# Performance work log

Measured on AMD Instinct MI355X. Metric: run time of the kernel, lower is better.

Reference implementation:

```python
import jax, jax.numpy as jnp
import numpy as np

B, M, E, K = 8, 256, 128, 16
H, A, R, RMS = 1024, 256, 1024, 512
NEG = -1e25


def setup_inputs() -> dict:
    key = jax.random.key(0)
    ks = jax.random.split(key, 12)
    inp = {
        "mention_reprs": jax.random.normal(ks[0], (B, M, H), jnp.float32),
        "entities": jax.random.randint(ks[1], (B, E, K), 0, M),
        "entity_masks": jax.random.randint(ks[2], (B, E, K), 0, 2, dtype=jnp.int32),
        "relation_memory": jax.random.normal(ks[3], (R, RMS), jnp.float32),
        # GatedMILAttention params
        "Wv": jax.random.normal(ks[4], (A, H), jnp.float32) / np.sqrt(H),
        "bv": jnp.zeros((A,), jnp.float32),
        "Wu": jax.random.normal(ks[5], (A, H), jnp.float32) / np.sqrt(H),
        "bu": jnp.zeros((A,), jnp.float32),
        "Wa": jax.random.normal(ks[6], (1, A), jnp.float32) / np.sqrt(A),
        "ba": jnp.zeros((1,), jnp.float32),
        # relation memory read linear: Linear(RMS, H)
        "Wr": jax.random.normal(ks[7], (H, RMS), jnp.float32) / np.sqrt(RMS),
        "br": jnp.zeros((H,), jnp.float32),
        # output linear: Linear(H + RMS, H)
        "Wo": jax.random.normal(ks[8], (H, H + RMS), jnp.float32) / np.sqrt(H + RMS),
        "bo": jnp.zeros((H,), jnp.float32),
    }
    return inp


def reference(mention_reprs, entities, entity_masks, relation_memory,
              Wv, bv, Wu, bu, Wa, ba, Wr, br, Wo, bo):
    # gather mention clusters: [B, E, K, H]
    clusters = jax.vmap(lambda m, e: m[e])(mention_reprs, entities)
    # gated MIL attention
    aV = jnp.tanh(jnp.einsum('bekh,ah->beka', clusters, Wv) + bv)
    aU = jax.nn.sigmoid(jnp.einsum('bekh,ah->beka', clusters, Wu) + bu)
    logits = jnp.einsum('beka,oa->beko', aV * aU, Wa) + ba  # [B,E,K,1]
    mask = entity_masks[..., None].astype(bool)
    logits = jnp.where(mask, logits, NEG)
    a = jax.nn.softmax(logits, axis=2)
    # weighted pooling over mentions: [B, E, H]
    entity_reprs = jnp.sum(a * clusters, axis=2)
    # relation memory read (memory detached for the read projection)
    s_w = jax.lax.stop_gradient(relation_memory) @ Wr.T + br        # [R, H]
    s = jnp.einsum('beh,rh->ber', entity_reprs, s_w)                # [B, E, R]
    s = jnp.einsum('ber,rm->bem', s, relation_memory)               # [B, E, RMS]
    out = jnp.concatenate([entity_reprs, s], axis=-1) @ Wo.T + bo   # [B, E, H]
    return out  # dropout is identity at inference
```

## Files before the change

kernel.cpp:

```cpp
#include <hip/hip_runtime.h>
#include <cstdint>
#include <cstddef>

#define NEG_ (-1e25f)

typedef __bf16 bf16x8 __attribute__((ext_vector_type(8)));
typedef float  f32x4  __attribute__((ext_vector_type(4)));
typedef short  s16x8  __attribute__((ext_vector_type(8)));
typedef const __attribute__((address_space(1))) void* gas_t;
typedef __attribute__((address_space(3))) void* las_t;

#define MFMA16 __builtin_amdgcn_mfma_f32_16x16x32_bf16

__device__ __forceinline__ short f2bf(float f) {
  union { float f; unsigned u; } v; v.f = f;
  unsigned r = v.u + 0x7fffu + ((v.u >> 16) & 1u);
  return (short)(r >> 16);
}

__device__ __forceinline__ s16x8 cvt8(const float* s) {
  bf16x8 r;
  #pragma unroll
  for (int j = 0; j < 8; ++j) r[j] = (__bf16)s[j];
  union { bf16x8 b; s16x8 s; } u; u.b = r; return u.s;
}

template <int NT>
__device__ void fgemm64(const float* __restrict__ A, long lda,
                        const float* __restrict__ B, long ldb,
                        short* __restrict__ C, int ldc, int m0, int n0,
                        short* lds) {
  const int tid = threadIdx.x, wave = tid >> 6, lane = tid & 63;
  const int quad = lane >> 4, l16 = lane & 15;
  const int wm = (wave & 1) * 32, wn = (wave >> 1) * 32;
  const int srow = tid >> 2, scol = (tid & 3) * 8;
  const float* Ag = A + (long)(m0 + srow) * lda + scol;
  const float* Bg = B + (long)(n0 + srow) * ldb + scol;
  short* As = lds; short* Bs = lds + 2048;
  float ra[8], rb[8];
  auto gload = [&](int kt) {
    long k = (long)kt * 32;
    *(float4*)(ra)     = *(const float4*)(Ag + k);
    *(float4*)(ra + 4) = *(const float4*)(Ag + k + 4);
    *(float4*)(rb)     = *(const float4*)(Bg + k);
    *(float4*)(rb + 4) = *(const float4*)(Bg + k + 4);
  };
  f32x4 acc[2][2] = {};
  gload(0);
  for (int kt = 0; kt < NT; ++kt) {
    *(s16x8*)&As[srow * 32 + scol] = cvt8(ra);
    *(s16x8*)&Bs[srow * 32 + scol] = cvt8(rb);
    __syncthreads();
    if (kt + 1 < NT) gload(kt + 1);
    bf16x8 a0 = *(const bf16x8*)&As[(wm + l16) * 32 + quad * 8];
    bf16x8 a1 = *(const bf16x8*)&As[(wm + 16 + l16) * 32 + quad * 8];
    bf16x8 b0 = *(const bf16x8*)&Bs[(wn + l16) * 32 + quad * 8];
    bf16x8 b1 = *(const bf16x8*)&Bs[(wn + 16 + l16) * 32 + quad * 8];
    acc[0][0] = MFMA16(a0, b0, acc[0][0], 0, 0, 0);
    acc[0][1] = MFMA16(a0, b1, acc[0][1], 0, 0, 0);
    acc[1][0] = MFMA16(a1, b0, acc[1][0], 0, 0, 0);
    acc[1][1] = MFMA16(a1, b1, acc[1][1], 0, 0, 0);
    __syncthreads();
  }
  #pragma unroll
  for (int i = 0; i < 2; ++i)
    #pragma unroll
    for (int j = 0; j < 2; ++j) {
      int col = n0 + wn + j * 16 + l16;
      #pragma unroll
      for (int r = 0; r < 4; ++r) {
        int row = m0 + wm + i * 16 + quad * 4 + r;
        C[(long)row * ldc + col] = f2bf(acc[i][j][r]);
      }
    }
}

template <int EPI>
__device__ void bgemm64(const short* __restrict__ A, int lda,
                        const short* __restrict__ B, int ldb,
                        void* __restrict__ C, int ldc, int NT, int m0, int n0,
                        const float* __restrict__ e0, const float* __restrict__ e1,
                        const float* __restrict__ e2, short* lds) {
  short* As = lds;
  short* Bs = lds + 4 * 2048;
  const int tid = threadIdx.x;
  const int wave = tid >> 6, lane = tid & 63;
  const int quad = lane >> 4, l16 = lane & 15;
  const int wm = (wave & 1) * 32, wn = (wave >> 1) * 32;
  const int srow = tid >> 2, scol = (tid & 3) * 8;
  const short* Ag = A + (long)(m0 + srow) * lda + scol;
  const short* Bg = B + (long)(n0 + srow) * ldb + scol;
  const int ldsoff = wave * 512;
  auto issue = [&](int kt) {
    int buf = kt & 3; int ko = kt * 32;
    __builtin_amdgcn_global_load_lds((gas_t)(Ag + ko), (las_t)(As + buf * 2048 + ldsoff), 16, 0, 0);
    __builtin_amdgcn_global_load_lds((gas_t)(Bg + ko), (las_t)(Bs + buf * 2048 + ldsoff), 16, 0, 0);
  };
  f32x4 acc[2][2] = {};
  issue(0); issue(1); issue(2);
  for (int kt = 0; kt < NT; ++kt) {
    if (kt + 3 < NT) issue(kt + 3);
    int ahead = NT - 1 - kt; if (ahead > 3) ahead = 3;
    if (ahead == 3)      asm volatile("s_waitcnt vmcnt(6)" ::: "memory");
    else if (ahead == 2) asm volatile("s_waitcnt vmcnt(4)" ::: "memory");
    else if (ahead == 1) asm volatile("s_waitcnt vmcnt(2)" ::: "memory");
    else                 asm volatile("s_waitcnt vmcnt(0)" ::: "memory");
    asm volatile("s_barrier" ::: "memory");
    const short* as = As + (kt & 3) * 2048;
    const short* bs = Bs + (kt & 3) * 2048;
    bf16x8 a0 = *(const bf16x8*)&as[(wm + l16) * 32 + quad * 8];
    bf16x8 a1 = *(const bf16x8*)&as[(wm + 16 + l16) * 32 + quad * 8];
    bf16x8 b0 = *(const bf16x8*)&bs[(wn + l16) * 32 + quad * 8];
    bf16x8 b1 = *(const bf16x8*)&bs[(wn + 16 + l16) * 32 + quad * 8];
    acc[0][0] = MFMA16(a0, b0, acc[0][0], 0, 0, 0);
    acc[0][1] = MFMA16(a0, b1, acc[0][1], 0, 0, 0);
    acc[1][0] = MFMA16(a1, b0, acc[1][0], 0, 0, 0);
    acc[1][1] = MFMA16(a1, b1, acc[1][1], 0, 0, 0);
    asm volatile("s_barrier" ::: "memory");
  }
  #pragma unroll
  for (int i = 0; i < 2; ++i)
    #pragma unroll
    for (int j = 0; j < 2; ++j) {
      int col = n0 + wn + j * 16 + l16;
      #pragma unroll
      for (int r = 0; r < 4; ++r) {
        int row = m0 + wm + i * 16 + quad * 4 + r;
        float v = acc[i][j][r];
        if constexpr (EPI == 1) {
          v += e0[(long)row * 1536 + col];
          ((short*)C)[(long)row * ldc + col] = f2bf(v);
        } else {
          v += e0[col] + e1[row] * e2[col];
          ((float*)C)[(long)row * ldc + col] = v;
        }
      }
    }
}

__device__ void vu_tile(int mi, int ni, const float* __restrict__ X,
                        const float* __restrict__ Wv, const float* __restrict__ Wu,
                        const float* __restrict__ bv, const float* __restrict__ bu,
                        const float* __restrict__ Wa, float* __restrict__ wpart,
                        short* lds, float* red) {
  const int tid = threadIdx.x, wave = tid >> 6, lane = tid & 63;
  const int quad = lane >> 4, l16 = lane & 15;
  const int wm = (wave & 1) * 16, wn = (wave >> 1) * 32;
  const int m0 = mi * 32, n0 = ni * 64;
  const int srow = tid >> 2, scol = (tid & 3) * 8;
  short* As = lds;
  short* Bvs = lds + 1024;
  short* Bus = lds + 3072;
  const float* Ag  = X  + (long)(m0 + srow) * 1024 + scol;
  const float* Bvg = Wv + (long)(n0 + srow) * 1024 + scol;
  const float* Bug = Wu + (long)(n0 + srow) * 1024 + scol;
  float ra[8], rv[8], ru[8];
  auto gload = [&](int kt) {
    long k = (long)kt * 32;
    if (tid < 128) {
      *(float4*)(ra)     = *(const float4*)(Ag + k);
      *(float4*)(ra + 4) = *(const float4*)(Ag + k + 4);
    }
    *(float4*)(rv)     = *(const float4*)(Bvg + k);
    *(float4*)(rv + 4) = *(const float4*)(Bvg + k + 4);
    *(float4*)(ru)     = *(const float4*)(Bug + k);
    *(float4*)(ru + 4) = *(const float4*)(Bug + k + 4);
  };
  f32x4 accv[2] = {}, accu[2] = {};
  gload(0);
  for (int kt = 0; kt < 32; ++kt) {
    if (tid < 128) *(s16x8*)&As[srow * 32 + scol] = cvt8(ra);
    *(s16x8*)&Bvs[srow * 32 + scol] = cvt8(rv);
    *(s16x8*)&Bus[srow * 32 + scol] = cvt8(ru);
    __syncthreads();
    if (kt + 1 < 32) gload(kt + 1);
    bf16x8 af = *(const bf16x8*)&As[(wm + l16) * 32 + quad * 8];
    bf16x8 v0 = *(const bf16x8*)&Bvs[(wn + l16) * 32 + quad * 8];
    bf16x8 v1 = *(const bf16x8*)&Bvs[(wn + 16 + l16) * 32 + quad * 8];
    bf16x8 u0 = *(const bf16x8*)&Bus[(wn + l16) * 32 + quad * 8];
    bf16x8 u1 = *(const bf16x8*)&Bus[(wn + 16 + l16) * 32 + quad * 8];
    accv[0] = MFMA16(af, v0, accv[0], 0, 0, 0);
    accv[1] = MFMA16(af, v1, accv[1], 0, 0, 0);
    accu[0] = MFMA16(af, u0, accu[0], 0, 0, 0);
    accu[1] = MFMA16(af, u1, accu[1], 0, 0, 0);
    __syncthreads();
  }
  float wsum[4] = {0.f, 0.f, 0.f, 0.f};
  #pragma unroll
  for (int j = 0; j < 2; ++j) {
    int col = n0 + wn + j * 16 + l16;
    float bvc = bv[col], buc = bu[col], wac = Wa[col];
    #pragma unroll
    for (int r = 0; r < 4; ++r) {
      float vv = tanhf(accv[j][r] + bvc);
      float uu = accu[j][r] + buc;
      wsum[r] += (vv / (1.0f + expf(-uu))) * wac;
    }
  }
  #pragma unroll
  for (int r = 0; r < 4; ++r) {
    float s = wsum[r];
    s += __shfl_down(s, 8, 16);
    s += __shfl_down(s, 4, 16);
    s += __shfl_down(s, 2, 16);
    s += __shfl_down(s, 1, 16);
    if (l16 == 0) red[(wave >> 1) * 32 + wm + quad * 4 + r] = s;
  }
  __syncthreads();
  if (tid < 32) wpart[ni * 2048 + m0 + tid] = red[tid] + red[32 + tid];
}

__device__ void softmax_entity(int be, const float* __restrict__ ment,
    const int* __restrict__ ents, const int* __restrict__ msk,
    const float* __restrict__ wpart, const float* __restrict__ br,
    short* __restrict__ erb, float* __restrict__ cf,
    float* sm_a, int* sm_idx, float* sm_red) {
  const int b = be >> 7;
  const int tid = threadIdx.x;
  __syncthreads();
  if (tid < 16) {
    int idx = ents[be * 16 + tid];
    sm_idx[tid] = idx;
    int j = (b << 8) + idx;
    float lw = wpart[j] + wpart[2048 + j] + wpart[4096 + j] + wpart[6144 + j];
    sm_a[tid] = msk[be * 16 + tid] ? lw : NEG_;
  }
  __syncthreads();
  if (tid == 0) {
    float mx = sm_a[0];
    #pragma unroll
    for (int k = 1; k < 16; ++k) mx = fmaxf(mx, sm_a[k]);
    float e[16], s = 0.f;
    #pragma unroll
    for (int k = 0; k < 16; ++k) { e[k] = expf(sm_a[k] - mx); s += e[k]; }
    float inv = 1.0f / s;
    #pragma unroll
    for (int k = 0; k < 16; ++k) sm_a[k] = e[k] * inv;
  }
  __syncthreads();
  const float* Xr = ment + ((long)b << 18);
  const int h0 = tid * 4;
  float ax = 0.f, ay = 0.f, az = 0.f, aw = 0.f;
  #pragma unroll
  for (int k = 0; k < 16; ++k) {
    float ak = sm_a[k];
    float4 xv = *(const float4*)&Xr[(long)sm_idx[k] * 1024 + h0];
    ax += ak * xv.x; ay += ak * xv.y; az += ak * xv.z; aw += ak * xv.w;
  }
  short* er = erb + (long)be * 1024 + h0;
  er[0] = f2bf(ax); er[1] = f2bf(ay); er[2] = f2bf(az); er[3] = f2bf(aw);
  float4 brv = *(const float4*)&br[h0];
  float c = ax * brv.x + ay * brv.y + az * brv.z + aw * brv.w;
  #pragma unroll
  for (int off = 32; off > 0; off >>= 1) c += __shfl_down(c, off);
  if ((tid & 63) == 0) sm_red[tid >> 6] = c;
  __syncthreads();
  if (tid == 0) cf[be] = sm_red[0] + sm_red[1] + sm_red[2] + sm_red[3];
}

__global__ __launch_bounds__(256) void k1(
    const float* __restrict__ rm, const float* __restrict__ ment,
    const float* __restrict__ Wv, const float* __restrict__ Wu,
    const float* __restrict__ bv, const float* __restrict__ bu,
    const float* __restrict__ Wa, const float* __restrict__ Wr,
    const float* __restrict__ Wo, short* __restrict__ swTb,
    short* __restrict__ Ub, float* __restrict__ wpart) {
  __shared__ short lds[5120];
  __shared__ float red[64];
  const int blk = blockIdx.x;
  if (blk < 256) {
    fgemm64<16>(Wr, 512, rm, 512, swTb, 1024, (blk >> 4) * 64, (blk & 15) * 64, lds);
  } else if (blk < 512) {
    int q = blk - 256;
    fgemm64<16>(Wo + 1024, 1536, rm, 512, Ub, 1024, (q >> 4) * 64, (q & 15) * 64, lds);
  } else {
    int q = blk - 512;
    vu_tile(q & 63, q >> 6, ment, Wv, Wu, bv, bu, Wa, wpart, lds, red);
  }
}

__global__ __launch_bounds__(256) void k2(
    const short* __restrict__ Ub, const short* __restrict__ swTb,
    const float* __restrict__ Wo, const float* __restrict__ ment,
    const int* __restrict__ ents, const int* __restrict__ msk,
    const float* __restrict__ wpart, const float* __restrict__ br,
    short* __restrict__ Weffb, float* __restrict__ gw2,
    short* __restrict__ erb, float* __restrict__ cf) {
  __shared__ short lds[16384];
  __shared__ float sm_a[16];
  __shared__ int   sm_idx[16];
  __shared__ float sm_red[4];
  const int blk = blockIdx.x, tid = threadIdx.x;
  if (blk < 256) {
    bgemm64<1>(Ub, 1024, swTb, 1024, Weffb, 1024, 32,
               (blk >> 4) * 64, (blk & 15) * 64, Wo, nullptr, nullptr, lds);
  } else if (blk < 260) {
    int row = (blk - 256) * 256 + tid;
    const short* u = Ub + (long)row * 1024;
    float s = 0.f;
    for (int k = 0; k < 1024; k += 8) {
      s16x8 v = *(const s16x8*)&u[k];
      union { s16x8 s; bf16x8 b; } w; w.s = v;
      #pragma unroll
      for (int j = 0; j < 8; ++j) s += (float)w.b[j];
    }
    gw2[row] = s;
  } else {
    int s4 = (blk - 260) * 4;
    for (int e = 0; e < 4; ++e)
      softmax_entity(s4 + e, ment, ents, msk, wpart, br, erb, cf,
                     sm_a, sm_idx, sm_red);
  }
}

__global__ __launch_bounds__(256) void k3(
    const short* __restrict__ erb, const short* __restrict__ Weffb,
    const float* __restrict__ bo, const float* __restrict__ cf,
    const float* __restrict__ gw2, float* __restrict__ out) {
  __shared__ short lds[16384];
  const int blk = blockIdx.x;
  bgemm64<2>(erb, 1024, Weffb, 1024, out, 1024, 32,
             (blk >> 4) * 64, (blk & 15) * 64, bo, cf, gw2, lds);
}

extern "C" void kernel_launch(void* const* d_in, const int* in_sizes, int n_in,
                              void* d_out, int out_size, void* d_ws, size_t ws_size,
                              hipStream_t stream) {
  const float* ment = (const float*)d_in[0];
  const int*   ents = (const int*)d_in[1];
  const int*   msk  = (const int*)d_in[2];
  const float* rm   = (const float*)d_in[3];
  const float* Wv   = (const float*)d_in[4];
  const float* bv   = (const float*)d_in[5];
  const float* Wu   = (const float*)d_in[6];
  const float* bu   = (const float*)d_in[7];
  const float* Wa   = (const float*)d_in[8];
  const float* Wr   = (const float*)d_in[10];
  const float* br   = (const float*)d_in[11];
  const float* Wo   = (const float*)d_in[12];
  const float* bo   = (const float*)d_in[13];
  float* out = (float*)d_out;

  char* p = (char*)d_ws;
  auto alloc = [&](size_t bytes) {
    void* q = (void*)p; p += (bytes + 255) & ~(size_t)255; return q;
  };
  short* swTb  = (short*)alloc((size_t)1024 * 1024 * 2);
  short* Ub    = (short*)alloc((size_t)1024 * 1024 * 2);
  short* Weffb = (short*)alloc((size_t)1024 * 1024 * 2);
  short* erb   = (short*)alloc((size_t)1024 * 1024 * 2);
  float* wpart = (float*)alloc((size_t)4 * 2048 * 4);
  float* cf    = (float*)alloc((size_t)1024 * 4);
  float* gw2   = (float*)alloc((size_t)1024 * 4);

  k1<<<768, 256, 0, stream>>>(rm, ment, Wv, Wu, bv, bu, Wa, Wr, Wo,
                              swTb, Ub, wpart);
  k2<<<516, 256, 0, stream>>>(Ub, swTb, Wo, ment, ents, msk, wpart, br,
                              Weffb, gw2, erb, cf);
  k3<<<256, 256, 0, stream>>>(erb, Weffb, bo, cf, gw2, out);
}
```

Baseline: 141.8 us.

## Double-buffer LDS in fp32 GEMM tiles and drop per-iteration trailing barrier

```diff
diff --git a/kernel.cpp b/kernel.cpp
--- a/kernel.cpp
+++ b/kernel.cpp
@@ -36,22 +36,24 @@
   const int srow = tid >> 2, scol = (tid & 3) * 8;
   const float* Ag = A + (long)(m0 + srow) * lda + scol;
   const float* Bg = B + (long)(n0 + srow) * ldb + scol;
-  short* As = lds; short* Bs = lds + 2048;
-  float ra[8], rb[8];
-  auto gload = [&](int kt) {
+  float ra[2][8], rb[2][8];
+  auto gload = [&](int kt, int s) {
     long k = (long)kt * 32;
-    *(float4*)(ra)     = *(const float4*)(Ag + k);
-    *(float4*)(ra + 4) = *(const float4*)(Ag + k + 4);
-    *(float4*)(rb)     = *(const float4*)(Bg + k);
-    *(float4*)(rb + 4) = *(const float4*)(Bg + k + 4);
+    *(float4*)(ra[s])     = *(const float4*)(Ag + k);
+    *(float4*)(ra[s] + 4) = *(const float4*)(Ag + k + 4);
+    *(float4*)(rb[s])     = *(const float4*)(Bg + k);
+    *(float4*)(rb[s] + 4) = *(const float4*)(Bg + k + 4);
   };
   f32x4 acc[2][2] = {};
-  gload(0);
+  gload(0, 0); gload(1, 1);
   for (int kt = 0; kt < NT; ++kt) {
-    *(s16x8*)&As[srow * 32 + scol] = cvt8(ra);
-    *(s16x8*)&Bs[srow * 32 + scol] = cvt8(rb);
+    const int s = kt & 1;
+    short* As = lds + s * 4096;
+    short* Bs = As + 2048;
+    *(s16x8*)&As[srow * 32 + scol] = cvt8(ra[s]);
+    *(s16x8*)&Bs[srow * 32 + scol] = cvt8(rb[s]);
     __syncthreads();
-    if (kt + 1 < NT) gload(kt + 1);
+    if (kt + 2 < NT) gload(kt + 2, s);
     bf16x8 a0 = *(const bf16x8*)&As[(wm + l16) * 32 + quad * 8];
     bf16x8 a1 = *(const bf16x8*)&As[(wm + 16 + l16) * 32 + quad * 8];
     bf16x8 b0 = *(const bf16x8*)&Bs[(wn + l16) * 32 + quad * 8];
@@ -60,7 +62,6 @@
     acc[0][1] = MFMA16(a0, b1, acc[0][1], 0, 0, 0);
     acc[1][0] = MFMA16(a1, b0, acc[1][0], 0, 0, 0);
     acc[1][1] = MFMA16(a1, b1, acc[1][1], 0, 0, 0);
-    __syncthreads();
   }
   #pragma unroll
   for (int i = 0; i < 2; ++i)
@@ -99,13 +100,12 @@
   f32x4 acc[2][2] = {};
   issue(0); issue(1); issue(2);
   for (int kt = 0; kt < NT; ++kt) {
+    int rem = NT - 1 - kt;
+    if (rem >= 2)      asm volatile("s_waitcnt vmcnt(4)" ::: "memory");
+    else if (rem == 1) asm volatile("s_waitcnt vmcnt(2)" ::: "memory");
+    else               asm volatile("s_waitcnt vmcnt(0)" ::: "memory");
+    asm volatile("s_barrier" ::: "memory");
     if (kt + 3 < NT) issue(kt + 3);
-    int ahead = NT - 1 - kt; if (ahead > 3) ahead = 3;
-    if (ahead == 3)      asm volatile("s_waitcnt vmcnt(6)" ::: "memory");
-    else if (ahead == 2) asm volatile("s_waitcnt vmcnt(4)" ::: "memory");
-    else if (ahead == 1) asm volatile("s_waitcnt vmcnt(2)" ::: "memory");
-    else                 asm volatile("s_waitcnt vmcnt(0)" ::: "memory");
-    asm volatile("s_barrier" ::: "memory");
     const short* as = As + (kt & 3) * 2048;
     const short* bs = Bs + (kt & 3) * 2048;
     bf16x8 a0 = *(const bf16x8*)&as[(wm + l16) * 32 + quad * 8];
@@ -116,7 +116,6 @@
     acc[0][1] = MFMA16(a0, b1, acc[0][1], 0, 0, 0);
     acc[1][0] = MFMA16(a1, b0, acc[1][0], 0, 0, 0);
     acc[1][1] = MFMA16(a1, b1, acc[1][1], 0, 0, 0);
-    asm volatile("s_barrier" ::: "memory");
   }
   #pragma unroll
   for (int i = 0; i < 2; ++i)
@@ -148,32 +147,33 @@
   const int wm = (wave & 1) * 16, wn = (wave >> 1) * 32;
   const int m0 = mi * 32, n0 = ni * 64;
   const int srow = tid >> 2, scol = (tid & 3) * 8;
-  short* As = lds;
-  short* Bvs = lds + 1024;
-  short* Bus = lds + 3072;
   const float* Ag  = X  + (long)(m0 + srow) * 1024 + scol;
   const float* Bvg = Wv + (long)(n0 + srow) * 1024 + scol;
   const float* Bug = Wu + (long)(n0 + srow) * 1024 + scol;
-  float ra[8], rv[8], ru[8];
-  auto gload = [&](int kt) {
+  float ra[2][8], rv[2][8], ru[2][8];
+  auto gload = [&](int kt, int s) {
     long k = (long)kt * 32;
     if (tid < 128) {
-      *(float4*)(ra)     = *(const float4*)(Ag + k);
-      *(float4*)(ra + 4) = *(const float4*)(Ag + k + 4);
-    }
-    *(float4*)(rv)     = *(const float4*)(Bvg + k);
-    *(float4*)(rv + 4) = *(const float4*)(Bvg + k + 4);
-    *(float4*)(ru)     = *(const float4*)(Bug + k);
-    *(float4*)(ru + 4) = *(const float4*)(Bug + k + 4);
+      *(float4*)(ra[s])     = *(const float4*)(Ag + k);
+      *(float4*)(ra[s] + 4) = *(const float4*)(Ag + k + 4);
+    }
+    *(float4*)(rv[s])     = *(const float4*)(Bvg + k);
+    *(float4*)(rv[s] + 4) = *(const float4*)(Bvg + k + 4);
+    *(float4*)(ru[s])     = *(const float4*)(Bug + k);
+    *(float4*)(ru[s] + 4) = *(const float4*)(Bug + k + 4);
   };
   f32x4 accv[2] = {}, accu[2] = {};
-  gload(0);
+  gload(0, 0); gload(1, 1);
   for (int kt = 0; kt < 32; ++kt) {
-    if (tid < 128) *(s16x8*)&As[srow * 32 + scol] = cvt8(ra);
-    *(s16x8*)&Bvs[srow * 32 + scol] = cvt8(rv);
-    *(s16x8*)&Bus[srow * 32 + scol] = cvt8(ru);
+    const int s = kt & 1;
+    short* As  = lds + s * 5120;
+    short* Bvs = As + 1024;
+    short* Bus = As + 3072;
+    if (tid < 128) *(s16x8*)&As[srow * 32 + scol] = cvt8(ra[s]);
+    *(s16x8*)&Bvs[srow * 32 + scol] = cvt8(rv[s]);
+    *(s16x8*)&Bus[srow * 32 + scol] = cvt8(ru[s]);
     __syncthreads();
-    if (kt + 1 < 32) gload(kt + 1);
+    if (kt + 2 < 32) gload(kt + 2, s);
     bf16x8 af = *(const bf16x8*)&As[(wm + l16) * 32 + quad * 8];
     bf16x8 v0 = *(const bf16x8*)&Bvs[(wn + l16) * 32 + quad * 8];
     bf16x8 v1 = *(const bf16x8*)&Bvs[(wn + 16 + l16) * 32 + quad * 8];
@@ -183,7 +183,6 @@
     accv[1] = MFMA16(af, v1, accv[1], 0, 0, 0);
     accu[0] = MFMA16(af, u0, accu[0], 0, 0, 0);
     accu[1] = MFMA16(af, u1, accu[1], 0, 0, 0);
-    __syncthreads();
   }
   float wsum[4] = {0.f, 0.f, 0.f, 0.f};
   #pragma unroll
@@ -265,7 +264,7 @@
     const float* __restrict__ Wa, const float* __restrict__ Wr,
     const float* __restrict__ Wo, short* __restrict__ swTb,
     short* __restrict__ Ub, float* __restrict__ wpart) {
-  __shared__ short lds[5120];
+  __shared__ short lds[10240];
   __shared__ float red[64];
   const int blk = blockIdx.x;
   if (blk < 256) {
```

New measurement: 187.8 us. 32.4% more time.
